# Performance work log

Measured on AMD Instinct MI355X. Metric: run time of the kernel, lower is better.

## Reference

```python
import jax, jax.numpy as jnp
import numpy as np

N_NODES = 30000
N_REL = 8
N_EDGES = 150000
EMB = 128
HID = 128
OUT = 256
HEADS = 4
RANK = 8
SCALE = 1.0
NEG_SLOPE = 0.2
LN_EPS = 1e-5


def setup_inputs():
    key = jax.random.key(0)
    ks = jax.random.split(key, 16)
    def nrm(k, shp, s=0.05):
        return jax.random.normal(k, shp, dtype=jnp.float32) * s
    d2 = HEADS * HID  # conv2 input dim = 512
    return {
        "entity_emb": nrm(ks[0], (N_NODES, EMB)),
        "A1": nrm(ks[1], (N_REL, EMB * RANK)),
        "B1": nrm(ks[2], (N_REL, EMB * RANK)),
        "W1": nrm(ks[3], (HEADS * HID, EMB)),
        "att_l1": nrm(ks[4], (1, HEADS, HID)),
        "att_r1": nrm(ks[5], (1, HEADS, HID)),
        "relb1": jnp.zeros((N_REL, HEADS), jnp.float32),
        "bias1": jnp.zeros((HEADS * HID,), jnp.float32),
        "A2": nrm(ks[6], (N_REL, d2 * RANK)),
        "B2": nrm(ks[7], (N_REL, d2 * RANK)),
        "W2": nrm(ks[8], (OUT, d2)),
        "att_l2": nrm(ks[9], (1, 1, OUT)),
        "att_r2": nrm(ks[10], (1, 1, OUT)),
        "relb2": jnp.zeros((N_REL, 1), jnp.float32),
        "bias2": jnp.zeros((OUT,), jnp.float32),
        "res_W": nrm(ks[11], (OUT, EMB)),
        "res_b": jnp.zeros((OUT,), jnp.float32),
        "ln_g": jnp.ones((OUT,), jnp.float32),
        "ln_b": jnp.zeros((OUT,), jnp.float32),
        "edge_index": jax.random.randint(ks[12], (2, N_EDGES), 0, N_NODES),
        "edge_type": jax.random.randint(ks[13], (N_EDGES,), 0, N_REL),
    }


def _rel_gat_conv(x, A, B, W, att_l, att_r, relb, bias, j_idx, i_idx, etype, heads, out_dim, concat):
    # x: [N,d]; A,B: [R, d*k]; W: [heads*out_dim, d]
    N, d = x.shape
    R = A.shape[0]
    k = RANK
    HC = heads * out_dim
    A3 = A.reshape(R, d, k)
    B3 = B.reshape(R, d, k)
    z_all = x @ W.T  # [N, HC] base linear (shared by z_i and z_j)
    # LoRA low-rank projection per (node, relation): P[n,r] = B_r^T x_n
    P = jnp.einsum('nd,rdk->nrk', x, B3)          # [N,R,k] (small)
    low = P[j_idx, etype]                          # [E,k]
    # Fused LoRA-through-lin: lin(scale*A_r B_r^T x) = scale * low @ (A_r^T W^T)
    M = jnp.einsum('rdk,hd->rkh', A3, W).reshape(R * k, HC)  # [R*k, HC]
    oh = jax.nn.one_hot(etype, R, dtype=x.dtype)   # [E,R]
    low_exp = (oh[:, :, None] * low[:, None, :]).reshape(-1, R * k)  # [E,R*k]
    z_j = (z_all[j_idx] + SCALE * (low_exp @ M)).reshape(-1, heads, out_dim)  # [E,H,C]
    z_i = z_all[i_idx].reshape(-1, heads, out_dim)                            # [E,H,C]
    alpha = (z_i * att_l).sum(-1) + (z_j * att_r).sum(-1) + relb[etype]       # [E,H]
    alpha = jax.nn.leaky_relu(alpha, NEG_SLOPE)
    # per-relation loop => softmax groups are (relation, target node)
    seg = etype * N + i_idx
    n_seg = R * N
    amax = jax.ops.segment_max(alpha, seg, num_segments=n_seg)
    ex = jnp.exp(alpha - amax[seg])
    den = jax.ops.segment_sum(ex, seg, num_segments=n_seg)
    alpha = ex / den[seg]
    msg = z_j * alpha[:, :, None]                  # [E,H,C]
    out = jax.ops.segment_sum(msg, i_idx, num_segments=N)  # [N,H,C]
    out = out.reshape(N, HC) if concat else out.mean(axis=1)
    return out + bias


def _forward(entity_emb, A1, B1, W1, att_l1, att_r1, relb1, bias1,
             A2, B2, W2, att_l2, att_r2, relb2, bias2,
             res_W, res_b, ln_g, ln_b, edge_index, edge_type):
    j_idx, i_idx = edge_index[0], edge_index[1]
    x0 = entity_emb
    x = _rel_gat_conv(x0, A1, B1, W1, att_l1, att_r1, relb1, bias1,
                      j_idx, i_idx, edge_type, HEADS, HID, True)
    x = jax.nn.elu(x)
    x = _rel_gat_conv(x, A2, B2, W2, att_l2, att_r2, relb2, bias2,
                      j_idx, i_idx, edge_type, 1, OUT, False)
    x = x + (x0 @ res_W.T + res_b)
    mu = x.mean(axis=-1, keepdims=True)
    var = ((x - mu) ** 2).mean(axis=-1, keepdims=True)
    return (x - mu) / jnp.sqrt(var + LN_EPS) * ln_g + ln_b


def reference(entity_emb, A1, B1, W1, att_l1, att_r1, relb1, bias1,
              A2, B2, W2, att_l2, att_r2, relb2, bias2,
              res_W, res_b, ln_g, ln_b, edge_index, edge_type):
    return _forward(entity_emb, A1, B1, W1, att_l1, att_r1, relb1, bias1,
                    A2, B2, W2, att_l2, att_r2, relb2, bias2,
                    res_W, res_b, ln_g, ln_b, edge_index, edge_type)
```

## Files before the change

kernel.cpp:

```cpp
#include <hip/hip_runtime.h>
#include <cstddef>

#define NRELS 8
#define EMB 128
#define HID 128
#define OUTD 256
#define HEADS 4
#define RANK 8
#define D2 512
#define KCAT 192
#define NEG_SLOPE 0.2f
#define LN_EPS 1e-5f

typedef short bf16x8 __attribute__((ext_vector_type(8)));
typedef float f32x4 __attribute__((ext_vector_type(4)));

__device__ __forceinline__ unsigned short f2bf(float f) {
  union { float f; unsigned u; } v; v.f = f;
  unsigned u = v.u;
  return (unsigned short)((u + 0x7fffu + ((u >> 16) & 1u)) >> 16);
}
__device__ __forceinline__ float bf2f(unsigned short u) {
  union { unsigned u; float f; } v; v.u = (unsigned)u << 16; return v.f;
}

#define GLOAD16(ldsp, gp) \
  __builtin_amdgcn_global_load_lds((const __attribute__((address_space(1))) unsigned int*)(gp), \
      (__attribute__((address_space(3))) unsigned int*)(ldsp), 16, 0, 0)

template<int ATT, int BIAS, int F32OUT>
__global__ __launch_bounds__(256) void gemm_tile(const unsigned short* __restrict__ A,
    const unsigned short* __restrict__ B, unsigned short* __restrict__ C,
    float* __restrict__ Cf, int M, int N, int K,
    const float* __restrict__ bias, const float* __restrict__ b1p,
    const float* __restrict__ attL, const float* __restrict__ attR,
    float* __restrict__ al, float* __restrict__ ar) {
  __shared__ unsigned short As[128 * 32];
  __shared__ unsigned short Bs[128 * 32];
  __shared__ float pL[2][128];
  __shared__ float pR[2][128];
  const int tid = threadIdx.x;
  const int wave = tid >> 6;
  const int lane = tid & 63;
  const int wm = wave & 1;
  const int wn = wave >> 1;
  const int r16 = lane & 15;
  const int quad = lane >> 4;
  const int bm = blockIdx.x * 128;
  const int bn = blockIdx.y * 128;
  const int lr = lane >> 2;
  const int lc = (((lane & 3) ^ ((lane >> 3) & 3))) * 8;
  int arow0 = bm + wave * 32 + lr;      if (arow0 >= M) arow0 = M - 1;
  int arow1 = bm + wave * 32 + 16 + lr; if (arow1 >= M) arow1 = M - 1;
  const unsigned short* Ag0 = A + (size_t)arow0 * K + lc;
  const unsigned short* Ag1 = A + (size_t)arow1 * K + lc;
  const unsigned short* Bg0 = B + (size_t)(bn + wave * 32 + lr) * K + lc;
  const unsigned short* Bg1 = B + (size_t)(bn + wave * 32 + 16 + lr) * K + lc;
  unsigned short* lA0 = As + wave * 1024;
  unsigned short* lA1 = As + wave * 1024 + 512;
  unsigned short* lB0 = Bs + wave * 1024;
  unsigned short* lB1 = Bs + wave * 1024 + 512;
  const int rsw = (quad ^ ((r16 >> 1) & 3)) * 8;
  f32x4 acc[4][4] = {};
  for (int k0 = 0; k0 < K; k0 += 32) {
    __syncthreads();
    GLOAD16(lA0, Ag0 + k0);
    GLOAD16(lA1, Ag1 + k0);
    GLOAD16(lB0, Bg0 + k0);
    GLOAD16(lB1, Bg1 + k0);
    __syncthreads();
    bf16x8 af[4], bfr[4];
#pragma unroll
    for (int mi = 0; mi < 4; ++mi)
      af[mi] = *(const bf16x8*)(As + (wm * 64 + mi * 16 + r16) * 32 + rsw);
#pragma unroll
    for (int ni = 0; ni < 4; ++ni)
      bfr[ni] = *(const bf16x8*)(Bs + (wn * 64 + ni * 16 + r16) * 32 + rsw);
#pragma unroll
    for (int mi = 0; mi < 4; ++mi)
#pragma unroll
      for (int ni = 0; ni < 4; ++ni)
        acc[mi][ni] = __builtin_amdgcn_mfma_f32_16x16x32_bf16(af[mi], bfr[ni], acc[mi][ni], 0, 0, 0);
  }
  float bcol[4];
  if (BIAS) {
#pragma unroll
    for (int ni = 0; ni < 4; ++ni) {
      int cn = bn + wn * 64 + ni * 16 + r16;
      bcol[ni] = bias[cn];
      if (F32OUT) bcol[ni] += b1p[cn];
    }
  }
#pragma unroll
  for (int mi = 0; mi < 4; ++mi)
#pragma unroll
    for (int ni = 0; ni < 4; ++ni)
#pragma unroll
      for (int r = 0; r < 4; ++r) {
        int row = bm + wm * 64 + mi * 16 + quad * 4 + r;
        if (row < M) {
          float v = acc[mi][ni][r];
          if (BIAS) v += bcol[ni];
          size_t idx = (size_t)row * N + bn + wn * 64 + ni * 16 + r16;
          if (F32OUT) Cf[idx] = v;
          else        C[idx] = f2bf(v);
        }
      }
  if (ATT) {
    float La[4], Ra[4];
#pragma unroll
    for (int ni = 0; ni < 4; ++ni) {
      int cn = bn + wn * 64 + ni * 16 + r16;
      La[ni] = attL[cn]; Ra[ni] = attR[cn];
    }
#pragma unroll
    for (int mi = 0; mi < 4; ++mi)
#pragma unroll
      for (int r = 0; r < 4; ++r) {
        float sl = 0.f, sr = 0.f;
#pragma unroll
        for (int ni = 0; ni < 4; ++ni) {
          sl = fmaf(acc[mi][ni][r], La[ni], sl);
          sr = fmaf(acc[mi][ni][r], Ra[ni], sr);
        }
#pragma unroll
        for (int o = 1; o < 16; o <<= 1) {
          sl += __shfl_xor(sl, o, 64);
          sr += __shfl_xor(sr, o, 64);
        }
        if (r16 == 0) {
          int rl = wm * 64 + mi * 16 + quad * 4 + r;
          pL[wn][rl] = sl; pR[wn][rl] = sr;
        }
      }
    __syncthreads();
    if (tid < 128) {
      int row = bm + tid;
      if (row < M) {
        float sl = pL[0][tid] + pL[1][tid];
        float sr = pR[0][tid] + pR[1][tid];
        if (ATT == 1) {
          al[(size_t)row * 4 + blockIdx.y] = sl;
          ar[(size_t)row * 4 + blockIdx.y] = sr;
        } else {
          al[(size_t)blockIdx.y * M + row] = sl;
          ar[(size_t)blockIdx.y * M + row] = sr;
        }
      }
    }
  }
}

__global__ __launch_bounds__(256) void gemm_bf16t(const unsigned short* __restrict__ A,
    const unsigned short* __restrict__ B, float* __restrict__ C, int M, int N, int K) {
  __shared__ unsigned short As[64][40];
  __shared__ unsigned short Bs[64][40];
  const int tid = threadIdx.x;
  const int wave = tid >> 6;
  const int lane = tid & 63;
  const int wm = wave & 1;
  const int wn = wave >> 1;
  const int r16 = lane & 15;
  const int quad = lane >> 4;
  const int bm = blockIdx.x * 64;
  const int bn = blockIdx.y * 64;
  const int srow = tid >> 2;
  const int schunk = tid & 3;
  int arow = bm + srow; if (arow >= M) arow = M - 1;
  const unsigned short* Ag = A + (size_t)arow * K + schunk * 8;
  const unsigned short* Bg = B + (size_t)(bn + srow) * K + schunk * 8;
  f32x4 acc[2][2] = {};
  for (int k0 = 0; k0 < K; k0 += 32) {
    bf16x8 av = *(const bf16x8*)(Ag + k0);
    bf16x8 bv = *(const bf16x8*)(Bg + k0);
    __syncthreads();
    *(bf16x8*)(&As[srow][schunk * 8]) = av;
    *(bf16x8*)(&Bs[srow][schunk * 8]) = bv;
    __syncthreads();
    bf16x8 af0 = *(const bf16x8*)(&As[wm * 32 + r16][quad * 8]);
    bf16x8 af1 = *(const bf16x8*)(&As[wm * 32 + 16 + r16][quad * 8]);
    bf16x8 bf0 = *(const bf16x8*)(&Bs[wn * 32 + r16][quad * 8]);
    bf16x8 bf1 = *(const bf16x8*)(&Bs[wn * 32 + 16 + r16][quad * 8]);
    acc[0][0] = __builtin_amdgcn_mfma_f32_16x16x32_bf16(af0, bf0, acc[0][0], 0, 0, 0);
    acc[0][1] = __builtin_amdgcn_mfma_f32_16x16x32_bf16(af0, bf1, acc[0][1], 0, 0, 0);
    acc[1][0] = __builtin_amdgcn_mfma_f32_16x16x32_bf16(af1, bf0, acc[1][0], 0, 0, 0);
    acc[1][1] = __builtin_amdgcn_mfma_f32_16x16x32_bf16(af1, bf1, acc[1][1], 0, 0, 0);
  }
#pragma unroll
  for (int mi = 0; mi < 2; ++mi)
#pragma unroll
    for (int ni = 0; ni < 2; ++ni)
#pragma unroll
      for (int r = 0; r < 4; ++r) {
        int row = bm + wm * 32 + mi * 16 + quad * 4 + r;
        if (row < M)
          C[(size_t)row * N + bn + wn * 32 + ni * 16 + r16] = acc[mi][ni][r];
      }
}

__global__ __launch_bounds__(256) void gemm_abt(const float* __restrict__ A,
    const float* __restrict__ B, float* __restrict__ C, int M, int N, int K) {
  __shared__ float As[32][64];
  __shared__ float Bs[32][64];
  const int tid = threadIdx.x;
  const int bm = blockIdx.y * 64;
  const int bn = blockIdx.x * 64;
  const int tx = tid & 15;
  const int ty = tid >> 4;
  const int lr = tid & 63;
  const int lq = tid >> 6;
  float acc[4][4] = {};
  for (int k0 = 0; k0 < K; k0 += 32) {
#pragma unroll
    for (int s = 0; s < 2; ++s) {
      const int q = lq + s * 4;
      const int gm = bm + lr;
      float4 va = make_float4(0.f, 0.f, 0.f, 0.f);
      if (gm < M) va = *(const float4*)(A + (size_t)gm * K + k0 + q * 4);
      As[q * 4 + 0][lr] = va.x; As[q * 4 + 1][lr] = va.y;
      As[q * 4 + 2][lr] = va.z; As[q * 4 + 3][lr] = va.w;
      const int gn = bn + lr;
      float4 vb = *(const float4*)(B + (size_t)gn * K + k0 + q * 4);
      Bs[q * 4 + 0][lr] = vb.x; Bs[q * 4 + 1][lr] = vb.y;
      Bs[q * 4 + 2][lr] = vb.z; Bs[q * 4 + 3][lr] = vb.w;
    }
    __syncthreads();
#pragma unroll
    for (int kk = 0; kk < 32; ++kk) {
      float a[4], b[4];
#pragma unroll
      for (int i2 = 0; i2 < 4; ++i2) { a[i2] = As[kk][ty * 4 + i2]; b[i2] = Bs[kk][tx * 4 + i2]; }
#pragma unroll
      for (int i2 = 0; i2 < 4; ++i2)
#pragma unroll
        for (int j2 = 0; j2 < 4; ++j2)
          acc[i2][j2] = fmaf(a[i2], b[j2], acc[i2][j2]);
    }
    __syncthreads();
  }
#pragma unroll
  for (int i2 = 0; i2 < 4; ++i2) {
    const int gm = bm + ty * 4 + i2;
    if (gm >= M) continue;
#pragma unroll
    for (int j2 = 0; j2 < 4; ++j2)
      C[(size_t)gm * N + bn + tx * 4 + j2] = acc[i2][j2];
  }
}

__global__ void prep_all(const float* __restrict__ x0, const float* __restrict__ W1,
    const float* __restrict__ W2, const float* __restrict__ res_W,
    const float* __restrict__ A1, const float* __restrict__ A2,
    const float* __restrict__ B1, const float* __restrict__ B2,
    unsigned short* __restrict__ x0b, unsigned short* __restrict__ Acat,
    unsigned short* __restrict__ W1b, unsigned short* __restrict__ W2b,
    unsigned short* __restrict__ RWcat,
    float* __restrict__ Amat1, float* __restrict__ Amat2,
    unsigned short* __restrict__ Bmat1b, unsigned short* __restrict__ Bmat2b, int nx0) {
  int idx = blockIdx.x * 256 + threadIdx.x;
  if (idx < nx0) { unsigned short b = f2bf(x0[idx]); x0b[idx] = b;
    Acat[(size_t)(idx >> 7) * KCAT + (idx & 127)] = b; return; } idx -= nx0;
  if (idx < D2 * EMB) { W1b[idx] = f2bf(W1[idx]); return; } idx -= D2 * EMB;
  if (idx < OUTD * D2) { W2b[idx] = f2bf(W2[idx]); return; } idx -= OUTD * D2;
  if (idx < OUTD * EMB) { RWcat[(size_t)(idx >> 7) * KCAT + (idx & 127)] = f2bf(res_W[idx]); return; } idx -= OUTD * EMB;
  if (idx < 64 * EMB) { int d = idx % EMB, rk = idx / EMB, k = rk & 7, r = rk >> 3;
    Amat1[idx] = A1[(size_t)r * EMB * RANK + (size_t)d * RANK + k]; return; } idx -= 64 * EMB;
  if (idx < 64 * D2) { int d = idx % D2, rk = idx / D2, k = rk & 7, r = rk >> 3;
    Amat2[idx] = A2[(size_t)r * D2 * RANK + (size_t)d * RANK + k]; return; } idx -= 64 * D2;
  if (idx < 64 * EMB) { int d = idx % EMB, rk = idx / EMB, k = rk & 7, r = rk >> 3;
    Bmat1b[idx] = f2bf(B1[(size_t)r * EMB * RANK + (size_t)d * RANK + k]); return; } idx -= 64 * EMB;
  if (idx < 64 * D2) { int d = idx % D2, rk = idx / D2, k = rk & 7, r = rk >> 3;
    Bmat2b[idx] = f2bf(B2[(size_t)r * D2 * RANK + (size_t)d * RANK + k]); }
}

__global__ void fold_att(const float* __restrict__ M1, const float* __restrict__ attR1,
                         const float* __restrict__ M2, const float* __restrict__ attR2,
                         float* __restrict__ Matt1, float* __restrict__ Matt2) {
  int t = threadIdx.x;
  if (blockIdx.x == 0) {
    int h = t & 3, rk = t >> 2;
    float s = 0.f;
    for (int c = 0; c < HID; ++c)
      s = fmaf(M1[(size_t)rk * D2 + h * HID + c], attR1[h * HID + c], s);
    Matt1[rk * 4 + h] = s;
  } else if (t < 64) {
    float s = 0.f;
    for (int c = 0; c < OUTD; ++c) s = fmaf(M2[(size_t)t * OUTD + c], attR2[c], s);
    Matt2[t] = s;
  }
}

__global__ void build_MT(const float* __restrict__ M1, const float* __restrict__ M2,
                         unsigned short* __restrict__ M1T, unsigned short* __restrict__ RWcat) {
  int idx = blockIdx.x * 256 + threadIdx.x;
  if (idx < 512 * 256) {
    int c = idx >> 8, s = idx & 255;
    int h = s >> 6, rk = s & 63;
    float v = ((c >> 7) == h) ? M1[(size_t)rk * D2 + c] : 0.f;
    M1T[idx] = f2bf(v);
  } else {
    idx -= 512 * 256;
    if (idx < 256 * 64) {
      int c = idx >> 6, rk = idx & 63;
      RWcat[(size_t)c * KCAT + 128 + rk] = f2bf(M2[(size_t)rk * OUTD + c]);
    }
  }
}

__global__ void hist_kernel(const int* __restrict__ ii, int* __restrict__ deg,
                            int* __restrict__ prepos, int E) {
  int e = blockIdx.x * blockDim.x + threadIdx.x;
  if (e < E) prepos[e] = atomicAdd(&deg[ii[e]], 1);
}

__global__ __launch_bounds__(1024) void exscan_kernel(const int* __restrict__ deg,
                                                      int* __restrict__ rowstart, int n) {
  __shared__ int wsum[16];
  int t = threadIdx.x;
  int lane = t & 63, wid = t >> 6;
  int carry = 0;
  for (int base = 0; base < n; base += 4096) {
    int i0 = base + t * 4;
    int v0 = 0, v1 = 0, v2 = 0, v3 = 0;
    if (i0 + 3 < n) {
      int4 vv = *(const int4*)(deg + i0);
      v0 = vv.x; v1 = vv.y; v2 = vv.z; v3 = vv.w;
    } else {
      if (i0 < n) v0 = deg[i0];
      if (i0 + 1 < n) v1 = deg[i0 + 1];
      if (i0 + 2 < n) v2 = deg[i0 + 2];
      if (i0 + 3 < n) v3 = deg[i0 + 3];
    }
    int tot = v0 + v1 + v2 + v3;
    int x = tot;
#pragma unroll
    for (int o = 1; o < 64; o <<= 1) {
      int y = __shfl_up(x, o, 64);
      if (lane >= o) x += y;
    }
    if (lane == 63) wsum[wid] = x;
    __syncthreads();
    if (t == 0) {
      int s = carry;
      for (int w2 = 0; w2 < 16; ++w2) { int tmp = wsum[w2]; wsum[w2] = s; s += tmp; }
      carry = s;
    }
    __syncthreads();
    int ex0 = x - tot + wsum[wid];
    if (i0 + 3 < n) {
      int4 ov; ov.x = ex0; ov.y = ex0 + v0; ov.z = ex0 + v0 + v1; ov.w = ex0 + v0 + v1 + v2;
      *(int4*)(rowstart + i0) = ov;
    } else {
      if (i0 < n) rowstart[i0] = ex0;
      if (i0 + 1 < n) rowstart[i0 + 1] = ex0 + v0;
      if (i0 + 2 < n) rowstart[i0 + 2] = ex0 + v0 + v1;
      if (i0 + 3 < n) rowstart[i0 + 3] = ex0 + v0 + v1 + v2;
    }
    __syncthreads();
  }
  if (t == 0) rowstart[n] = carry;
}

__global__ void edge_alpha1(const int* __restrict__ ji, const int* __restrict__ ii,
                            const int* __restrict__ et, const int* __restrict__ rowstart,
                            const int* __restrict__ prepos,
                            const float* __restrict__ P1,
                            const float* __restrict__ al1, const float* __restrict__ ar1,
                            const float* __restrict__ relb1, const float* __restrict__ Matt1,
                            float4* __restrict__ recs1, int E) {
  int e = blockIdx.x * blockDim.x + threadIdx.x;
  if (e >= E) return;
  int j = ji[e], i = ii[e], rt = et[e];
  float4 lo0 = *(const float4*)(P1 + (size_t)j * 64 + rt * 8);
  float4 lo1 = *(const float4*)(P1 + (size_t)j * 64 + rt * 8 + 4);
  float low[RANK] = {lo0.x, lo0.y, lo0.z, lo0.w, lo1.x, lo1.y, lo1.z, lo1.w};
  float4 ali = *(const float4*)(al1 + (size_t)i * 4);
  float4 arj = *(const float4*)(ar1 + (size_t)j * 4);
  float4 rb  = *(const float4*)(relb1 + rt * 4);
  float a0 = ali.x + arj.x + rb.x;
  float a1 = ali.y + arj.y + rb.y;
  float a2 = ali.z + arj.z + rb.z;
  float a3 = ali.w + arj.w + rb.w;
#pragma unroll
  for (int k = 0; k < RANK; ++k) {
    float4 mk = *(const float4*)(Matt1 + ((rt * 8 + k) << 2));
    a0 = fmaf(low[k], mk.x, a0); a1 = fmaf(low[k], mk.y, a1);
    a2 = fmaf(low[k], mk.z, a2); a3 = fmaf(low[k], mk.w, a3);
  }
  a0 = (a0 > 0.f) ? a0 : NEG_SLOPE * a0;
  a1 = (a1 > 0.f) ? a1 : NEG_SLOPE * a1;
  a2 = (a2 > 0.f) ? a2 : NEG_SLOPE * a2;
  a3 = (a3 > 0.f) ? a3 : NEG_SLOPE * a3;
  float e0 = expf(a0), e1 = expf(a1), e2 = expf(a2), e3 = expf(a3);
  float4* rp = recs1 + (size_t)(rowstart[i] + prepos[e]) * 4;
  rp[0] = make_float4(__int_as_float(j), e0, e1, e2);
  rp[1] = make_float4(e3, __int_as_float(rt), low[0], low[1]);
  rp[2] = make_float4(low[2], low[3], low[4], low[5]);
  rp[3] = make_float4(low[6], low[7], 0.f, 0.f);
}

__global__ __launch_bounds__(256) void qden1(float4* __restrict__ recs1,
    const int* __restrict__ rowstart, unsigned short* __restrict__ Q1b, int Nn) {
  __shared__ float denS[4][32];
  const int wid = threadIdx.x >> 6, lane = threadIdx.x & 63;
  const int i = blockIdx.x * 4 + wid;
  if (i >= Nn) return;
  const int rt_mine = lane >> 3, k = lane & 7;
  const int s0 = rowstart[i], deg = rowstart[i + 1] - s0;
  const float* rf = (const float*)recs1;
  float q0 = 0.f, q1 = 0.f, q2 = 0.f, q3 = 0.f;
  float d0 = 0.f, d1 = 0.f, d2 = 0.f, d3 = 0.f;
  float4 a0 = {}, a1 = {};
  float lw = 0.f;
  if (deg > 0) {
    a0 = recs1[(size_t)s0 * 4]; a1 = recs1[(size_t)s0 * 4 + 1];
    lw = rf[(size_t)s0 * 16 + 6 + k];
  }
  for (int p = 0; p < deg; ++p) {
    float4 b0 = a0, b1 = a1; float lwn = lw;
    if (p + 1 < deg) {
      b0 = recs1[(size_t)(s0 + p + 1) * 4]; b1 = recs1[(size_t)(s0 + p + 1) * 4 + 1];
      lwn = rf[(size_t)(s0 + p + 1) * 16 + 6 + k];
    }
    int rt = __float_as_int(a1.y);
    if (rt == rt_mine) {
      q0 = fmaf(a0.y, lw, q0); q1 = fmaf(a0.z, lw, q1);
      q2 = fmaf(a0.w, lw, q2); q3 = fmaf(a1.x, lw, q3);
      d0 += a0.y; d1 += a0.z; d2 += a0.w; d3 += a1.x;
    }
    a0 = b0; a1 = b1; lw = lwn;
  }
  float r0 = (d0 > 0.f) ? 1.f / d0 : 0.f;
  float r1 = (d1 > 0.f) ? 1.f / d1 : 0.f;
  float r2 = (d2 > 0.f) ? 1.f / d2 : 0.f;
  float r3 = (d3 > 0.f) ? 1.f / d3 : 0.f;
  size_t qb = (size_t)i * 256;
  Q1b[qb + lane]       = f2bf(q0 * r0);
  Q1b[qb + 64 + lane]  = f2bf(q1 * r1);
  Q1b[qb + 128 + lane] = f2bf(q2 * r2);
  Q1b[qb + 192 + lane] = f2bf(q3 * r3);
  if (k == 0) {
    denS[wid][rt_mine]      = r0;
    denS[wid][8 + rt_mine]  = r1;
    denS[wid][16 + rt_mine] = r2;
    denS[wid][24 + rt_mine] = r3;
  }
  for (int p = lane; p < deg; p += 64) {
    float4* rp = recs1 + (size_t)(s0 + p) * 4;
    float4 v0 = rp[0]; float4 v1 = rp[1];
    int rt = __float_as_int(v1.y);
    v0.y *= denS[wid][rt];      v0.z *= denS[wid][8 + rt];
    v0.w *= denS[wid][16 + rt]; v1.x *= denS[wid][24 + rt];
    rp[0] = v0; rp[1] = v1;
  }
}

__global__ __launch_bounds__(256) void node_agg1_lite(const float4* __restrict__ recs1,
    const int* __restrict__ rowstart, const unsigned short* __restrict__ z1b,
    const unsigned short* __restrict__ L1b, unsigned short* __restrict__ h1out, int Nn) {
  const int wid = threadIdx.x >> 6;
  const int lane = threadIdx.x & 63;
  const int i = blockIdx.x * 4 + wid;
  if (i >= Nn) return;
  const int s0 = rowstart[i];
  const int deg = rowstart[i + 1] - s0;
  const int c0 = lane * 8;
  const float* rf = (const float*)recs1;
  float acc[8] = {};
  float4 rc = {}, rn = {};
  float w3c = 0.f, w3n = 0.f;
  uint4 zc = {};
  if (deg > 0) {
    rc = recs1[(size_t)s0 * 4];
    w3c = rf[(size_t)s0 * 16 + 4];
    zc = *(const uint4*)(z1b + (size_t)__float_as_int(rc.x) * D2 + c0);
  }
  if (deg > 1) {
    rn = recs1[(size_t)(s0 + 1) * 4];
    w3n = rf[(size_t)(s0 + 1) * 16 + 4];
  }
  for (int p = 0; p < deg; ++p) {
    float4 r2 = rn; float w32 = w3n;
    uint4 zn = zc;
    if (p + 2 < deg) {
      r2 = recs1[(size_t)(s0 + p + 2) * 4];
      w32 = rf[(size_t)(s0 + p + 2) * 16 + 4];
    }
    if (p + 1 < deg)
      zn = *(const uint4*)(z1b + (size_t)__float_as_int(rn.x) * D2 + c0);
    float wlo = (lane & 16) ? rc.z : rc.y;
    float whi = (lane & 16) ? w3c : rc.w;
    float wt = (lane & 32) ? whi : wlo;
    acc[0] = fmaf(wt, bf2f((unsigned short)(zc.x & 0xffff)), acc[0]);
    acc[1] = fmaf(wt, bf2f((unsigned short)(zc.x >> 16)), acc[1]);
    acc[2] = fmaf(wt, bf2f((unsigned short)(zc.y & 0xffff)), acc[2]);
    acc[3] = fmaf(wt, bf2f((unsigned short)(zc.y >> 16)), acc[3]);
    acc[4] = fmaf(wt, bf2f((unsigned short)(zc.z & 0xffff)), acc[4]);
    acc[5] = fmaf(wt, bf2f((unsigned short)(zc.z >> 16)), acc[5]);
    acc[6] = fmaf(wt, bf2f((unsigned short)(zc.w & 0xffff)), acc[6]);
    acc[7] = fmaf(wt, bf2f((unsigned short)(zc.w >> 16)), acc[7]);
    rc = rn; w3c = w3n; rn = r2; w3n = w32; zc = zn;
  }
  uint4 lv = *(const uint4*)(L1b + (size_t)i * D2 + c0);
  unsigned lw[4] = {lv.x, lv.y, lv.z, lv.w};
  unsigned ov[4];
#pragma unroll
  for (int q = 0; q < 4; ++q) {
    float e0 = acc[2 * q]     + bf2f((unsigned short)(lw[q] & 0xffff));
    float e1 = acc[2 * q + 1] + bf2f((unsigned short)(lw[q] >> 16));
    e0 = e0 > 0.f ? e0 : expm1f(e0);
    e1 = e1 > 0.f ? e1 : expm1f(e1);
    ov[q] = (unsigned)f2bf(e0) | ((unsigned)f2bf(e1) << 16);
  }
  *(uint4*)(h1out + (size_t)i * D2 + c0) = make_uint4(ov[0], ov[1], ov[2], ov[3]);
}

__global__ void edge_alpha2(const int* __restrict__ ji, const int* __restrict__ ii,
                            const int* __restrict__ et, const int* __restrict__ rowstart,
                            const int* __restrict__ prepos,
                            const float* __restrict__ P2,
                            const float* __restrict__ al2, const float* __restrict__ ar2,
                            const float* __restrict__ relb2, const float* __restrict__ Matt2,
                            float4* __restrict__ recs2, int E, int Nn) {
  int e = blockIdx.x * blockDim.x + threadIdx.x;
  if (e >= E) return;
  int j = ji[e], i = ii[e], rt = et[e];
  float4 lo0 = *(const float4*)(P2 + (size_t)j * 64 + rt * 8);
  float4 lo1 = *(const float4*)(P2 + (size_t)j * 64 + rt * 8 + 4);
  float low[RANK] = {lo0.x, lo0.y, lo0.z, lo0.w, lo1.x, lo1.y, lo1.z, lo1.w};
  float a = al2[i] + al2[(size_t)Nn + i] + ar2[j] + ar2[(size_t)Nn + j] + relb2[rt];
#pragma unroll
  for (int k = 0; k < RANK; ++k) a = fmaf(low[k], Matt2[rt * RANK + k], a);
  a = (a > 0.f) ? a : NEG_SLOPE * a;
  float ex = expf(a);
  float4* rp = recs2 + (size_t)(rowstart[i] + prepos[e]) * 3;
  rp[0] = make_float4(__int_as_float(j), __int_as_float(rt), ex, low[0]);
  rp[1] = make_float4(low[1], low[2], low[3], low[4]);
  rp[2] = make_float4(low[5], low[6], low[7], 0.f);
}

__global__ __launch_bounds__(256) void qden2(float4* __restrict__ recs2,
    const int* __restrict__ rowstart, unsigned short* __restrict__ Acat, int Nn) {
  __shared__ float denS[4][NRELS];
  const int wid = threadIdx.x >> 6, lane = threadIdx.x & 63;
  const int i = blockIdx.x * 4 + wid;
  if (i >= Nn) return;
  const int rt_mine = lane >> 3, k = lane & 7;
  const int s0 = rowstart[i], deg = rowstart[i + 1] - s0;
  const float* rf = (const float*)recs2;
  float q = 0.f, d = 0.f;
  float4 a0 = {}; float lw = 0.f;
  if (deg > 0) { a0 = recs2[(size_t)s0 * 3]; lw = rf[(size_t)s0 * 12 + 3 + k]; }
  for (int p = 0; p < deg; ++p) {
    float4 b0 = a0; float lwn = lw;
    if (p + 1 < deg) {
      b0 = recs2[(size_t)(s0 + p + 1) * 3];
      lwn = rf[(size_t)(s0 + p + 1) * 12 + 3 + k];
    }
    int rt = __float_as_int(a0.y);
    if (rt == rt_mine) { q = fmaf(a0.z, lw, q); d += a0.z; }
    a0 = b0; lw = lwn;
  }
  float rd = (d > 0.f) ? 1.f / d : 0.f;
  Acat[(size_t)i * KCAT + 128 + lane] = f2bf(q * rd);
  if (k == 0) denS[wid][rt_mine] = rd;
  for (int p = lane; p < deg; p += 64) {
    float* ep = (float*)(recs2 + (size_t)(s0 + p) * 3);
    int rt = __float_as_int(ep[1]);
    ep[2] *= denS[wid][rt];
  }
}

__global__ __launch_bounds__(256) void node_agg2_lite(const float4* __restrict__ recs2,
    const int* __restrict__ rowstart, const unsigned short* __restrict__ z2b,
    const float* __restrict__ o2, const float* __restrict__ ln_g,
    const float* __restrict__ ln_b, float* __restrict__ y, int Nn) {
  const int wid = threadIdx.x >> 6;
  const int lane = threadIdx.x & 63;
  const int i = blockIdx.x * 4 + wid;
  if (i >= Nn) return;
  const int s0 = rowstart[i];
  const int deg = rowstart[i + 1] - s0;
  const int c0 = lane * 4;
  float acc[4] = {};
  float4 rc = {}, rn = {};
  uint2 zc = make_uint2(0u, 0u);
  if (deg > 0) {
    rc = recs2[(size_t)s0 * 3];
    zc = *(const uint2*)(z2b + (size_t)__float_as_int(rc.x) * OUTD + c0);
  }
  if (deg > 1) rn = recs2[(size_t)(s0 + 1) * 3];
  for (int p = 0; p < deg; ++p) {
    float4 r2 = rn;
    uint2 zn = zc;
    if (p + 2 < deg) r2 = recs2[(size_t)(s0 + p + 2) * 3];
    if (p + 1 < deg)
      zn = *(const uint2*)(z2b + (size_t)__float_as_int(rn.x) * OUTD + c0);
    float wt = rc.z;
    acc[0] = fmaf(wt, bf2f((unsigned short)(zc.x & 0xffff)), acc[0]);
    acc[1] = fmaf(wt, bf2f((unsigned short)(zc.x >> 16)), acc[1]);
    acc[2] = fmaf(wt, bf2f((unsigned short)(zc.y & 0xffff)), acc[2]);
    acc[3] = fmaf(wt, bf2f((unsigned short)(zc.y >> 16)), acc[3]);
    rc = rn; rn = r2; zc = zn;
  }
  float4 rsv = *(const float4*)(o2 + (size_t)i * OUTD + c0);
  float vv[4];
  vv[0] = acc[0] + rsv.x;
  vv[1] = acc[1] + rsv.y;
  vv[2] = acc[2] + rsv.z;
  vv[3] = acc[3] + rsv.w;
  float s = vv[0] + vv[1] + vv[2] + vv[3];
  for (int o = 32; o > 0; o >>= 1) s += __shfl_xor(s, o, 64);
  float mu = s * (1.f / OUTD);
  float q = 0.f;
#pragma unroll
  for (int k = 0; k < 4; ++k) { float d = vv[k] - mu; q += d * d; }
  for (int o = 32; o > 0; o >>= 1) q += __shfl_xor(q, o, 64);
  float rstd = rsqrtf(q * (1.f / OUTD) + LN_EPS);
  float4 g = *(const float4*)(ln_g + c0);
  float4 bb = *(const float4*)(ln_b + c0);
  float4 ov;
  ov.x = (vv[0] - mu) * rstd * g.x + bb.x;
  ov.y = (vv[1] - mu) * rstd * g.y + bb.y;
  ov.z = (vv[2] - mu) * rstd * g.z + bb.z;
  ov.w = (vv[3] - mu) * rstd * g.w + bb.w;
  *(float4*)(y + (size_t)i * OUTD + c0) = ov;
}

extern "C" void kernel_launch(void* const* d_in, const int* in_sizes, int n_in,
                              void* d_out, int out_size, void* d_ws, size_t ws_size,
                              hipStream_t stream) {
  const float* x0     = (const float*)d_in[0];
  const float* A1     = (const float*)d_in[1];
  const float* B1     = (const float*)d_in[2];
  const float* W1     = (const float*)d_in[3];
  const float* attL1  = (const float*)d_in[4];
  const float* attR1  = (const float*)d_in[5];
  const float* relb1  = (const float*)d_in[6];
  const float* bias1  = (const float*)d_in[7];
  const float* A2     = (const float*)d_in[8];
  const float* B2     = (const float*)d_in[9];
  const float* W2     = (const float*)d_in[10];
  const float* attL2  = (const float*)d_in[11];
  const float* attR2  = (const float*)d_in[12];
  const float* relb2  = (const float*)d_in[13];
  const float* bias2  = (const float*)d_in[14];
  const float* res_W  = (const float*)d_in[15];
  const float* res_b  = (const float*)d_in[16];
  const float* ln_g   = (const float*)d_in[17];
  const float* ln_b   = (const float*)d_in[18];
  const int*   eidx   = (const int*)d_in[19];
  const int*   etype  = (const int*)d_in[20];
  float* out = (float*)d_out;

  const int Nn = in_sizes[0] / EMB;
  const int E  = in_sizes[20];
  const int* ji = eidx;
  const int* ii = eidx + E;

  float* w = (float*)d_ws;
  size_t off = 0;
  float* o2    = w + off; off += (size_t)Nn * OUTD;
  float* P1    = w + off; off += (size_t)Nn * 64;
  float* P2    = w + off; off += (size_t)Nn * 64;
  float* M1    = w + off; off += 64 * D2;
  float* M2    = w + off; off += 64 * OUTD;
  float* Amat1 = w + off; off += 64 * EMB;
  float* Amat2 = w + off; off += 64 * D2;
  float* Matt1 = w + off; off += 64 * 4;
  float* Matt2 = w + off; off += 64;
  float* al1   = w + off; off += (size_t)Nn * 4;
  float* ar1   = w + off; off += (size_t)Nn * 4;
  float* al2   = w + off; off += (size_t)Nn * 2;
  float* ar2   = w + off; off += (size_t)Nn * 2;
  float4* recs1 = (float4*)(w + off); off += (size_t)E * 16;
  float4* recs2 = (float4*)(w + off); off += (size_t)E * 12;
  unsigned short* z1b    = (unsigned short*)(w + off); off += (size_t)Nn * D2 / 2;
  unsigned short* z2b    = (unsigned short*)(w + off); off += (size_t)Nn * OUTD / 2;
  unsigned short* x0b    = (unsigned short*)(w + off); off += (size_t)Nn * EMB / 2;
  unsigned short* h1b    = (unsigned short*)(w + off); off += (size_t)Nn * D2 / 2;
  unsigned short* W1b    = (unsigned short*)(w + off); off += (size_t)D2 * EMB / 2;
  unsigned short* W2b    = (unsigned short*)(w + off); off += (size_t)OUTD * D2 / 2;
  unsigned short* Bmat1b = (unsigned short*)(w + off); off += (size_t)64 * EMB / 2;
  unsigned short* Bmat2b = (unsigned short*)(w + off); off += (size_t)64 * D2 / 2;
  unsigned short* Acat   = (unsigned short*)(w + off); off += (size_t)Nn * KCAT / 2;
  unsigned short* RWcat  = (unsigned short*)(w + off); off += (size_t)OUTD * KCAT / 2;
  unsigned short* M1T    = (unsigned short*)(w + off); off += (size_t)512 * 256 / 2;
  int* ideg     = (int*)(w + off); off += (size_t)Nn;
  int* prepos   = (int*)(w + off); off += (size_t)E;
  int* rowstart = (int*)(w + off); off += (size_t)Nn + 1;
  (void)ws_size; (void)n_in; (void)out_size;

  unsigned short* Q1b = (unsigned short*)P1;
  unsigned short* L1b = (unsigned short*)o2;

  const int MT64 = (Nn + 63) / 64;
  const int MT128 = (Nn + 127) / 128;
  const int NB4 = (Nn + 3) / 4;

  (void)hipMemsetAsync(ideg, 0, (size_t)Nn * sizeof(int), stream);
  hist_kernel<<<(E + 255) / 256, 256, 0, stream>>>(ii, ideg, prepos, E);
  exscan_kernel<<<1, 1024, 0, stream>>>(ideg, rowstart, Nn);

  {
    int nx0 = Nn * EMB;
    int total = nx0 + D2 * EMB + OUTD * D2 + OUTD * EMB + 64 * EMB + 64 * D2 + 64 * EMB + 64 * D2;
    prep_all<<<(total + 255) / 256, 256, 0, stream>>>(x0, W1, W2, res_W, A1, A2, B1, B2,
        x0b, Acat, W1b, W2b, RWcat, Amat1, Amat2, Bmat1b, Bmat2b, nx0);
  }

  gemm_abt<<<dim3(D2 / 64, 1), 256, 0, stream>>>(Amat1, W1, M1, 64, D2, EMB);
  gemm_abt<<<dim3(OUTD / 64, 1), 256, 0, stream>>>(Amat2, W2, M2, 64, OUTD, D2);
  fold_att<<<2, 256, 0, stream>>>(M1, attR1, M2, attR2, Matt1, Matt2);
  build_MT<<<(512 * 256 + 256 * 64 + 255) / 256, 256, 0, stream>>>(M1, M2, M1T, RWcat);

  gemm_tile<1, 0, 0><<<dim3(MT128, D2 / 128), 256, 0, stream>>>(x0b, W1b, z1b, nullptr,
      Nn, D2, EMB, nullptr, nullptr, attL1, attR1, al1, ar1);
  gemm_bf16t<<<dim3(MT64, 1), 256, 0, stream>>>(x0b, Bmat1b, P1, Nn, 64, EMB);

  edge_alpha1<<<(E + 255) / 256, 256, 0, stream>>>(ji, ii, etype, rowstart, prepos, P1,
                                                   al1, ar1, relb1, Matt1, recs1, E);
  qden1<<<NB4, 256, 0, stream>>>(recs1, rowstart, Q1b, Nn);
  gemm_tile<0, 1, 0><<<dim3(MT128, D2 / 128), 256, 0, stream>>>(Q1b, M1T, L1b, nullptr,
      Nn, D2, 256, bias1, nullptr, nullptr, nullptr, nullptr, nullptr);
  node_agg1_lite<<<NB4, 256, 0, stream>>>(recs1, rowstart, z1b, L1b, h1b, Nn);

  gemm_tile<2, 0, 0><<<dim3(MT128, OUTD / 128), 256, 0, stream>>>(h1b, W2b, z2b, nullptr,
      Nn, OUTD, D2, nullptr, nullptr, attL2, attR2, al2, ar2);
  gemm_bf16t<<<dim3(MT64, 1), 256, 0, stream>>>(h1b, Bmat2b, P2, Nn, 64, D2);

  edge_alpha2<<<(E + 255) / 256, 256, 0, stream>>>(ji, ii, etype, rowstart, prepos, P2,
                                                   al2, ar2, relb2, Matt2, recs2, E, Nn);
  qden2<<<NB4, 256, 0, stream>>>(recs2, rowstart, Acat, Nn);
  gemm_tile<0, 1, 1><<<dim3(MT128, OUTD / 128), 256, 0, stream>>>(Acat, RWcat, nullptr, o2,
      Nn, OUTD, KCAT, bias2, res_b, nullptr, nullptr, nullptr, nullptr);
  node_agg2_lite<<<NB4, 256, 0, stream>>>(recs2, rowstart, z2b, o2, ln_g, ln_b, out, Nn);
}
```

Before: 401.9 us.

## Fuse LoRA projection GEMMs into main GEMMs, exploit block-diagonal M1T, merge prep kernels

Folds the per-node LoRA P projection into the z GEMM launch as an extra grid column, removing separate gemm_bf16t launches. Replaces the block-diagonal 512x256 M1T with a dense 512x64 per-head slice, indexed by a per-column A offset, which cuts the Q1 GEMM K from 256 to 64. Merges the two weight-folding GEMMs into one launch and fold_att with build_MT into one kernel. Deepens the gather prefetch pipeline in both aggregation kernels to two neighbours ahead. Risks include extra register pressure and load imbalance from the narrower P tile.

```diff
diff --git a/kernel.cpp b/kernel.cpp
--- a/kernel.cpp
+++ b/kernel.cpp
@@ -28,10 +28,11 @@
   __builtin_amdgcn_global_load_lds((const __attribute__((address_space(1))) unsigned int*)(gp), \
       (__attribute__((address_space(3))) unsigned int*)(ldsp), 16, 0, 0)
 
-template<int ATT, int BIAS, int F32OUT>
+template<int ATT, int BIAS, int F32OUT, int PB>
 __global__ __launch_bounds__(256) void gemm_tile(const unsigned short* __restrict__ A,
     const unsigned short* __restrict__ B, unsigned short* __restrict__ C,
-    float* __restrict__ Cf, int M, int N, int K,
+    float* __restrict__ Cf, const unsigned short* __restrict__ Bp,
+    float* __restrict__ Cp, int M, int N, int K, int lda, int aoffc,
     const float* __restrict__ bias, const float* __restrict__ b1p,
     const float* __restrict__ attL, const float* __restrict__ attR,
     float* __restrict__ al, float* __restrict__ ar) {
@@ -47,20 +48,60 @@
   const int r16 = lane & 15;
   const int quad = lane >> 4;
   const int bm = blockIdx.x * 128;
-  const int bn = blockIdx.y * 128;
   const int lr = lane >> 2;
   const int lc = (((lane & 3) ^ ((lane >> 3) & 3))) * 8;
+  const int rsw = (quad ^ ((r16 >> 1) & 3)) * 8;
   int arow0 = bm + wave * 32 + lr;      if (arow0 >= M) arow0 = M - 1;
   int arow1 = bm + wave * 32 + 16 + lr; if (arow1 >= M) arow1 = M - 1;
-  const unsigned short* Ag0 = A + (size_t)arow0 * K + lc;
-  const unsigned short* Ag1 = A + (size_t)arow1 * K + lc;
+  unsigned short* lA0 = As + wave * 1024;
+  unsigned short* lA1 = As + wave * 1024 + 512;
+
+  if (PB && blockIdx.y == (int)gridDim.y - 1) {
+    const unsigned short* Ag0 = A + (size_t)arow0 * lda + lc;
+    const unsigned short* Ag1 = A + (size_t)arow1 * lda + lc;
+    const unsigned short* Bg = Bp + (size_t)(wave * 16 + lr) * K + lc;
+    unsigned short* lBp = Bs + wave * 512;
+    f32x4 accp[4][2] = {};
+    for (int k0 = 0; k0 < K; k0 += 32) {
+      __syncthreads();
+      GLOAD16(lA0, Ag0 + k0);
+      GLOAD16(lA1, Ag1 + k0);
+      GLOAD16(lBp, Bg + k0);
+      __syncthreads();
+      bf16x8 af[4], bfr[2];
+#pragma unroll
+      for (int mi = 0; mi < 4; ++mi)
+        af[mi] = *(const bf16x8*)(As + (wm * 64 + mi * 16 + r16) * 32 + rsw);
+#pragma unroll
+      for (int ni = 0; ni < 2; ++ni)
+        bfr[ni] = *(const bf16x8*)(Bs + (wn * 32 + ni * 16 + r16) * 32 + rsw);
+#pragma unroll
+      for (int mi = 0; mi < 4; ++mi)
+#pragma unroll
+        for (int ni = 0; ni < 2; ++ni)
+          accp[mi][ni] = __builtin_amdgcn_mfma_f32_16x16x32_bf16(af[mi], bfr[ni], accp[mi][ni], 0, 0, 0);
+    }
+#pragma unroll
+    for (int mi = 0; mi < 4; ++mi)
+#pragma unroll
+      for (int ni = 0; ni < 2; ++ni)
+#pragma unroll
+        for (int r = 0; r < 4; ++r) {
+          int row = bm + wm * 64 + mi * 16 + quad * 4 + r;
+          if (row < M)
+            Cp[(size_t)row * 64 + wn * 32 + ni * 16 + r16] = accp[mi][ni][r];
+        }
+    return;
+  }
+
+  const int bn = blockIdx.y * 128;
+  const unsigned short* Abase = A + (size_t)blockIdx.y * aoffc;
+  const unsigned short* Ag0 = Abase + (size_t)arow0 * lda + lc;
+  const unsigned short* Ag1 = Abase + (size_t)arow1 * lda + lc;
   const unsigned short* Bg0 = B + (size_t)(bn + wave * 32 + lr) * K + lc;
   const unsigned short* Bg1 = B + (size_t)(bn + wave * 32 + 16 + lr) * K + lc;
-  unsigned short* lA0 = As + wave * 1024;
-  unsigned short* lA1 = As + wave * 1024 + 512;
   unsigned short* lB0 = Bs + wave * 1024;
   unsigned short* lB1 = Bs + wave * 1024 + 512;
-  const int rsw = (quad ^ ((r16 >> 1) & 3)) * 8;
   f32x4 acc[4][4] = {};
   for (int k0 = 0; k0 < K; k0 += 32) {
     __syncthreads();
@@ -151,60 +192,15 @@
   }
 }
 
-__global__ __launch_bounds__(256) void gemm_bf16t(const unsigned short* __restrict__ A,
-    const unsigned short* __restrict__ B, float* __restrict__ C, int M, int N, int K) {
-  __shared__ unsigned short As[64][40];
-  __shared__ unsigned short Bs[64][40];
-  const int tid = threadIdx.x;
-  const int wave = tid >> 6;
-  const int lane = tid & 63;
-  const int wm = wave & 1;
-  const int wn = wave >> 1;
-  const int r16 = lane & 15;
-  const int quad = lane >> 4;
-  const int bm = blockIdx.x * 64;
-  const int bn = blockIdx.y * 64;
-  const int srow = tid >> 2;
-  const int schunk = tid & 3;
-  int arow = bm + srow; if (arow >= M) arow = M - 1;
-  const unsigned short* Ag = A + (size_t)arow * K + schunk * 8;
-  const unsigned short* Bg = B + (size_t)(bn + srow) * K + schunk * 8;
-  f32x4 acc[2][2] = {};
-  for (int k0 = 0; k0 < K; k0 += 32) {
-    bf16x8 av = *(const bf16x8*)(Ag + k0);
-    bf16x8 bv = *(const bf16x8*)(Bg + k0);
-    __syncthreads();
-    *(bf16x8*)(&As[srow][schunk * 8]) = av;
-    *(bf16x8*)(&Bs[srow][schunk * 8]) = bv;
-    __syncthreads();
-    bf16x8 af0 = *(const bf16x8*)(&As[wm * 32 + r16][quad * 8]);
-    bf16x8 af1 = *(const bf16x8*)(&As[wm * 32 + 16 + r16][quad * 8]);
-    bf16x8 bf0 = *(const bf16x8*)(&Bs[wn * 32 + r16][quad * 8]);
-    bf16x8 bf1 = *(const bf16x8*)(&Bs[wn * 32 + 16 + r16][quad * 8]);
-    acc[0][0] = __builtin_amdgcn_mfma_f32_16x16x32_bf16(af0, bf0, acc[0][0], 0, 0, 0);
-    acc[0][1] = __builtin_amdgcn_mfma_f32_16x16x32_bf16(af0, bf1, acc[0][1], 0, 0, 0);
-    acc[1][0] = __builtin_amdgcn_mfma_f32_16x16x32_bf16(af1, bf0, acc[1][0], 0, 0, 0);
-    acc[1][1] = __builtin_amdgcn_mfma_f32_16x16x32_bf16(af1, bf1, acc[1][1], 0, 0, 0);
-  }
-#pragma unroll
-  for (int mi = 0; mi < 2; ++mi)
-#pragma unroll
-    for (int ni = 0; ni < 2; ++ni)
-#pragma unroll
-      for (int r = 0; r < 4; ++r) {
-        int row = bm + wm * 32 + mi * 16 + quad * 4 + r;
-        if (row < M)
-          C[(size_t)row * N + bn + wn * 32 + ni * 16 + r16] = acc[mi][ni][r];
-      }
-}
-
-__global__ __launch_bounds__(256) void gemm_abt(const float* __restrict__ A,
-    const float* __restrict__ B, float* __restrict__ C, int M, int N, int K) {
+__global__ __launch_bounds__(256) void gemm_abt2(const float* __restrict__ Amat1,
+    const float* __restrict__ W1, float* __restrict__ M1o,
+    const float* __restrict__ Amat2, const float* __restrict__ W2, float* __restrict__ M2o) {
+  const float* A; const float* B; float* C; int N, K, bn;
+  if (blockIdx.x < D2 / 64) { A = Amat1; B = W1; C = M1o; N = D2; K = EMB; bn = blockIdx.x * 64; }
+  else { A = Amat2; B = W2; C = M2o; N = OUTD; K = D2; bn = (blockIdx.x - D2 / 64) * 64; }
   __shared__ float As[32][64];
   __shared__ float Bs[32][64];
   const int tid = threadIdx.x;
-  const int bm = blockIdx.y * 64;
-  const int bn = blockIdx.x * 64;
   const int tx = tid & 15;
   const int ty = tid >> 4;
   const int lr = tid & 63;
@@ -214,13 +210,10 @@
 #pragma unroll
     for (int s = 0; s < 2; ++s) {
       const int q = lq + s * 4;
-      const int gm = bm + lr;
-      float4 va = make_float4(0.f, 0.f, 0.f, 0.f);
-      if (gm < M) va = *(const float4*)(A + (size_t)gm * K + k0 + q * 4);
+      float4 va = *(const float4*)(A + (size_t)lr * K + k0 + q * 4);
       As[q * 4 + 0][lr] = va.x; As[q * 4 + 1][lr] = va.y;
       As[q * 4 + 2][lr] = va.z; As[q * 4 + 3][lr] = va.w;
-      const int gn = bn + lr;
-      float4 vb = *(const float4*)(B + (size_t)gn * K + k0 + q * 4);
+      float4 vb = *(const float4*)(B + (size_t)(bn + lr) * K + k0 + q * 4);
       Bs[q * 4 + 0][lr] = vb.x; Bs[q * 4 + 1][lr] = vb.y;
       Bs[q * 4 + 2][lr] = vb.z; Bs[q * 4 + 3][lr] = vb.w;
     }
@@ -239,13 +232,10 @@
     __syncthreads();
   }
 #pragma unroll
-  for (int i2 = 0; i2 < 4; ++i2) {
-    const int gm = bm + ty * 4 + i2;
-    if (gm >= M) continue;
+  for (int i2 = 0; i2 < 4; ++i2)
 #pragma unroll
     for (int j2 = 0; j2 < 4; ++j2)
-      C[(size_t)gm * N + bn + tx * 4 + j2] = acc[i2][j2];
-  }
+      C[(size_t)(ty * 4 + i2) * N + bn + tx * 4 + j2] = acc[i2][j2];
 }
 
 __global__ void prep_all(const float* __restrict__ x0, const float* __restrict__ W1,
@@ -273,38 +263,24 @@
     Bmat2b[idx] = f2bf(B2[(size_t)r * D2 * RANK + (size_t)d * RANK + k]); }
 }
 
-__global__ void fold_att(const float* __restrict__ M1, const float* __restrict__ attR1,
-                         const float* __restrict__ M2, const float* __restrict__ attR2,
-                         float* __restrict__ Matt1, float* __restrict__ Matt2) {
-  int t = threadIdx.x;
-  if (blockIdx.x == 0) {
-    int h = t & 3, rk = t >> 2;
+__global__ void fold_build(const float* __restrict__ M1, const float* __restrict__ M2,
+                           const float* __restrict__ attR1, const float* __restrict__ attR2,
+                           unsigned short* __restrict__ M1T2, unsigned short* __restrict__ RWcat,
+                           float* __restrict__ Matt1, float* __restrict__ Matt2) {
+  int idx = blockIdx.x * 256 + threadIdx.x;
+  if (idx < 512 * 64) { int c = idx >> 6, rk = idx & 63;
+    M1T2[idx] = f2bf(M1[(size_t)rk * D2 + c]); return; } idx -= 512 * 64;
+  if (idx < 256 * 64) { int c = idx >> 6, rk = idx & 63;
+    RWcat[(size_t)c * KCAT + 128 + rk] = f2bf(M2[(size_t)rk * OUTD + c]); return; } idx -= 256 * 64;
+  if (idx < 256) { int h = idx & 3, rk = idx >> 2;
     float s = 0.f;
     for (int c = 0; c < HID; ++c)
       s = fmaf(M1[(size_t)rk * D2 + h * HID + c], attR1[h * HID + c], s);
-    Matt1[rk * 4 + h] = s;
-  } else if (t < 64) {
+    Matt1[rk * 4 + h] = s; return; } idx -= 256;
+  if (idx < 64) {
     float s = 0.f;
-    for (int c = 0; c < OUTD; ++c) s = fmaf(M2[(size_t)t * OUTD + c], attR2[c], s);
-    Matt2[t] = s;
-  }
-}
-
-__global__ void build_MT(const float* __restrict__ M1, const float* __restrict__ M2,
-                         unsigned short* __restrict__ M1T, unsigned short* __restrict__ RWcat) {
-  int idx = blockIdx.x * 256 + threadIdx.x;
-  if (idx < 512 * 256) {
-    int c = idx >> 8, s = idx & 255;
-    int h = s >> 6, rk = s & 63;
-    float v = ((c >> 7) == h) ? M1[(size_t)rk * D2 + c] : 0.f;
-    M1T[idx] = f2bf(v);
-  } else {
-    idx -= 512 * 256;
-    if (idx < 256 * 64) {
-      int c = idx >> 6, rk = idx & 63;
-      RWcat[(size_t)c * KCAT + 128 + rk] = f2bf(M2[(size_t)rk * OUTD + c]);
-    }
-  }
+    for (int c = 0; c < OUTD; ++c) s = fmaf(M2[(size_t)idx * OUTD + c], attR2[c], s);
+    Matt2[idx] = s; }
 }
 
 __global__ void hist_kernel(const int* __restrict__ ii, int* __restrict__ deg,
@@ -467,39 +443,31 @@
   const int c0 = lane * 8;
   const float* rf = (const float*)recs1;
   float acc[8] = {};
-  float4 rc = {}, rn = {};
-  float w3c = 0.f, w3n = 0.f;
-  uint4 zc = {};
-  if (deg > 0) {
-    rc = recs1[(size_t)s0 * 4];
-    w3c = rf[(size_t)s0 * 16 + 4];
-    zc = *(const uint4*)(z1b + (size_t)__float_as_int(rc.x) * D2 + c0);
-  }
-  if (deg > 1) {
-    rn = recs1[(size_t)(s0 + 1) * 4];
-    w3n = rf[(size_t)(s0 + 1) * 16 + 4];
-  }
+  float4 r0 = {}, r1 = {}, r2 = {};
+  float w0 = 0.f, w1 = 0.f, w2 = 0.f;
+  uint4 za = {}, zb = {};
+  if (deg > 0) { r0 = recs1[(size_t)s0 * 4]; w0 = rf[(size_t)s0 * 16 + 4];
+    za = *(const uint4*)(z1b + (size_t)__float_as_int(r0.x) * D2 + c0); }
+  if (deg > 1) { r1 = recs1[(size_t)(s0 + 1) * 4]; w1 = rf[(size_t)(s0 + 1) * 16 + 4];
+    zb = *(const uint4*)(z1b + (size_t)__float_as_int(r1.x) * D2 + c0); }
+  if (deg > 2) { r2 = recs1[(size_t)(s0 + 2) * 4]; w2 = rf[(size_t)(s0 + 2) * 16 + 4]; }
   for (int p = 0; p < deg; ++p) {
-    float4 r2 = rn; float w32 = w3n;
-    uint4 zn = zc;
-    if (p + 2 < deg) {
-      r2 = recs1[(size_t)(s0 + p + 2) * 4];
-      w32 = rf[(size_t)(s0 + p + 2) * 16 + 4];
-    }
-    if (p + 1 < deg)
-      zn = *(const uint4*)(z1b + (size_t)__float_as_int(rn.x) * D2 + c0);
-    float wlo = (lane & 16) ? rc.z : rc.y;
-    float whi = (lane & 16) ? w3c : rc.w;
+    float4 r3 = r2; float w3 = w2; uint4 zn = zb;
+    if (p + 3 < deg) { r3 = recs1[(size_t)(s0 + p + 3) * 4];
+                       w3 = rf[(size_t)(s0 + p + 3) * 16 + 4]; }
+    if (p + 2 < deg) zn = *(const uint4*)(z1b + (size_t)__float_as_int(r2.x) * D2 + c0);
+    float wlo = (lane & 16) ? r0.z : r0.y;
+    float whi = (lane & 16) ? w0 : r0.w;
     float wt = (lane & 32) ? whi : wlo;
-    acc[0] = fmaf(wt, bf2f((unsigned short)(zc.x & 0xffff)), acc[0]);
-    acc[1] = fmaf(wt, bf2f((unsigned short)(zc.x >> 16)), acc[1]);
-    acc[2] = fmaf(wt, bf2f((unsigned short)(zc.y & 0xffff)), acc[2]);
-    acc[3] = fmaf(wt, bf2f((unsigned short)(zc.y >> 16)), acc[3]);
-    acc[4] = fmaf(wt, bf2f((unsigned short)(zc.z & 0xffff)), acc[4]);
-    acc[5] = fmaf(wt, bf2f((unsigned short)(zc.z >> 16)), acc[5]);
-    acc[6] = fmaf(wt, bf2f((unsigned short)(zc.w & 0xffff)), acc[6]);
-    acc[7] = fmaf(wt, bf2f((unsigned short)(zc.w >> 16)), acc[7]);
-    rc = rn; w3c = w3n; rn = r2; w3n = w32; zc = zn;
+    acc[0] = fmaf(wt, bf2f((unsigned short)(za.x & 0xffff)), acc[0]);
+    acc[1] = fmaf(wt, bf2f((unsigned short)(za.x >> 16)), acc[1]);
+    acc[2] = fmaf(wt, bf2f((unsigned short)(za.y & 0xffff)), acc[2]);
+    acc[3] = fmaf(wt, bf2f((unsigned short)(za.y >> 16)), acc[3]);
+    acc[4] = fmaf(wt, bf2f((unsigned short)(za.z & 0xffff)), acc[4]);
+    acc[5] = fmaf(wt, bf2f((unsigned short)(za.z >> 16)), acc[5]);
+    acc[6] = fmaf(wt, bf2f((unsigned short)(za.w & 0xffff)), acc[6]);
+    acc[7] = fmaf(wt, bf2f((unsigned short)(za.w >> 16)), acc[7]);
+    r0 = r1; w0 = w1; r1 = r2; w1 = w2; r2 = r3; w2 = w3; za = zb; zb = zn;
   }
   uint4 lv = *(const uint4*)(L1b + (size_t)i * D2 + c0);
   unsigned lw[4] = {lv.x, lv.y, lv.z, lv.w};
@@ -583,25 +551,25 @@
   const int deg = rowstart[i + 1] - s0;
   const int c0 = lane * 4;
   float acc[4] = {};
-  float4 rc = {}, rn = {};
-  uint2 zc = make_uint2(0u, 0u);
-  if (deg > 0) {
-    rc = recs2[(size_t)s0 * 3];
-    zc = *(const uint2*)(z2b + (size_t)__float_as_int(rc.x) * OUTD + c0);
-  }
-  if (deg > 1) rn = recs2[(size_t)(s0 + 1) * 3];
+  float4 r0 = {}, r1 = {}, r2 = {};
+  uint2 za = make_uint2(0u, 0u), zb = make_uint2(0u, 0u);
+  if (deg > 0) { r0 = recs2[(size_t)s0 * 3];
+    za = *(const uint2*)(z2b + (size_t)__float_as_int(r0.x) * OUTD + c0); }
+  if (deg > 1) { r1 = recs2[(size_t)(s0 + 1) * 3];
+    zb = *(const uint2*)(z2b + (size_t)__float_as_int(r1.x) * OUTD + c0); }
+  if (deg > 2) r2 = recs2[(size_t)(s0 + 2) * 3];
   for (int p = 0; p < deg; ++p) {
-    float4 r2 = rn;
-    uint2 zn = zc;
-    if (p + 2 < deg) r2 = recs2[(size_t)(s0 + p + 2) * 3];
-    if (p + 1 < deg)
-      zn = *(const uint2*)(z2b + (size_t)__float_as_int(rn.x) * OUTD + c0);
-    float wt = rc.z;
-    acc[0] = fmaf(wt, bf2f((unsigned short)(zc.x & 0xffff)), acc[0]);
-    acc[1] = fmaf(wt, bf2f((unsigned short)(zc.x >> 16)), acc[1]);
-    acc[2] = fmaf(wt, bf2f((unsigned short)(zc.y & 0xffff)), acc[2]);
-    acc[3] = fmaf(wt, bf2f((unsigned short)(zc.y >> 16)), acc[3]);
-    rc = rn; rn = r2; zc = zn;
+    float4 r3 = r2;
+    uint2 zn = zb;
+    if (p + 3 < deg) r3 = recs2[(size_t)(s0 + p + 3) * 3];
+    if (p + 2 < deg)
+      zn = *(const uint2*)(z2b + (size_t)__float_as_int(r2.x) * OUTD + c0);
+    float wt = r0.z;
+    acc[0] = fmaf(wt, bf2f((unsigned short)(za.x & 0xffff)), acc[0]);
+    acc[1] = fmaf(wt, bf2f((unsigned short)(za.x >> 16)), acc[1]);
+    acc[2] = fmaf(wt, bf2f((unsigned short)(za.y & 0xffff)), acc[2]);
+    acc[3] = fmaf(wt, bf2f((unsigned short)(za.y >> 16)), acc[3]);
+    r0 = r1; r1 = r2; r2 = r3; za = zb; zb = zn;
   }
   float4 rsv = *(const float4*)(o2 + (size_t)i * OUTD + c0);
   float vv[4];
@@ -685,7 +653,7 @@
   unsigned short* Bmat2b = (unsigned short*)(w + off); off += (size_t)64 * D2 / 2;
   unsigned short* Acat   = (unsigned short*)(w + off); off += (size_t)Nn * KCAT / 2;
   unsigned short* RWcat  = (unsigned short*)(w + off); off += (size_t)OUTD * KCAT / 2;
-  unsigned short* M1T    = (unsigned short*)(w + off); off += (size_t)512 * 256 / 2;
+  unsigned short* M1T2   = (unsigned short*)(w + off); off += (size_t)512 * 64 / 2;
   int* ideg     = (int*)(w + off); off += (size_t)Nn;
   int* prepos   = (int*)(w + off); off += (size_t)E;
   int* rowstart = (int*)(w + off); off += (size_t)Nn + 1;
@@ -694,7 +662,6 @@
   unsigned short* Q1b = (unsigned short*)P1;
   unsigned short* L1b = (unsigned short*)o2;
 
-  const int MT64 = (Nn + 63) / 64;
   const int MT128 = (Nn + 127) / 128;
   const int NB4 = (Nn + 3) / 4;
 
@@ -709,30 +676,27 @@
         x0b, Acat, W1b, W2b, RWcat, Amat1, Amat2, Bmat1b, Bmat2b, nx0);
   }
 
-  gemm_abt<<<dim3(D2 / 64, 1), 256, 0, stream>>>(Amat1, W1, M1, 64, D2, EMB);
-  gemm_abt<<<dim3(OUTD / 64, 1), 256, 0, stream>>>(Amat2, W2, M2, 64, OUTD, D2);
-  fold_att<<<2, 256, 0, stream>>>(M1, attR1, M2, attR2, Matt1, Matt2);
-  build_MT<<<(512 * 256 + 256 * 64 + 255) / 256, 256, 0, stream>>>(M1, M2, M1T, RWcat);
-
-  gemm_tile<1, 0, 0><<<dim3(MT128, D2 / 128), 256, 0, stream>>>(x0b, W1b, z1b, nullptr,
-      Nn, D2, EMB, nullptr, nullptr, attL1, attR1, al1, ar1);
-  gemm_bf16t<<<dim3(MT64, 1), 256, 0, stream>>>(x0b, Bmat1b, P1, Nn, 64, EMB);
+  gemm_abt2<<<dim3(D2 / 64 + OUTD / 64, 1), 256, 0, stream>>>(Amat1, W1, M1, Amat2, W2, M2);
+  fold_build<<<(512 * 64 + 256 * 64 + 256 + 64 + 255) / 256, 256, 0, stream>>>(
+      M1, M2, attR1, attR2, M1T2, RWcat, Matt1, Matt2);
+
+  gemm_tile<1, 0, 0, 1><<<dim3(MT128, D2 / 128 + 1), 256, 0, stream>>>(x0b, W1b, z1b, nullptr,
+      Bmat1b, P1, Nn, D2, EMB, EMB, 0, nullptr, nullptr, attL1, attR1, al1, ar1);
 
   edge_alpha1<<<(E + 255) / 256, 256, 0, stream>>>(ji, ii, etype, rowstart, prepos, P1,
                                                    al1, ar1, relb1, Matt1, recs1, E);
   qden1<<<NB4, 256, 0, stream>>>(recs1, rowstart, Q1b, Nn);
-  gemm_tile<0, 1, 0><<<dim3(MT128, D2 / 128), 256, 0, stream>>>(Q1b, M1T, L1b, nullptr,
-      Nn, D2, 256, bias1, nullptr, nullptr, nullptr, nullptr, nullptr);
+  gemm_tile<0, 1, 0, 0><<<dim3(MT128, D2 / 128), 256, 0, stream>>>(Q1b, M1T2, L1b, nullptr,
+      nullptr, nullptr, Nn, D2, 64, 256, 64, bias1, nullptr, nullptr, nullptr, nullptr, nullptr);
   node_agg1_lite<<<NB4, 256, 0, stream>>>(recs1, rowstart, z1b, L1b, h1b, Nn);
 
-  gemm_tile<2, 0, 0><<<dim3(MT128, OUTD / 128), 256, 0, stream>>>(h1b, W2b, z2b, nullptr,
-      Nn, OUTD, D2, nullptr, nullptr, attL2, attR2, al2, ar2);
-  gemm_bf16t<<<dim3(MT64, 1), 256, 0, stream>>>(h1b, Bmat2b, P2, Nn, 64, D2);
+  gemm_tile<2, 0, 0, 1><<<dim3(MT128, OUTD / 128 + 1), 256, 0, stream>>>(h1b, W2b, z2b, nullptr,
+      Bmat2b, P2, Nn, OUTD, D2, D2, 0, nullptr, nullptr, attL2, attR2, al2, ar2);
 
   edge_alpha2<<<(E + 255) / 256, 256, 0, stream>>>(ji, ii, etype, rowstart, prepos, P2,
                                                    al2, ar2, relb2, Matt2, recs2, E, Nn);
   qden2<<<NB4, 256, 0, stream>>>(recs2, rowstart, Acat, Nn);
-  gemm_tile<0, 1, 1><<<dim3(MT128, OUTD / 128), 256, 0, stream>>>(Acat, RWcat, nullptr, o2,
-      Nn, OUTD, KCAT, bias2, res_b, nullptr, nullptr, nullptr, nullptr);
+  gemm_tile<0, 1, 1, 0><<<dim3(MT128, OUTD / 128), 256, 0, stream>>>(Acat, RWcat, nullptr, o2,
+      nullptr, nullptr, Nn, OUTD, KCAT, KCAT, 0, bias2, res_b, nullptr, nullptr, nullptr, nullptr);
   node_agg2_lite<<<NB4, 256, 0, stream>>>(recs2, rowstart, z2b, o2, ln_g, ln_b, out, Nn);
 }
```

Measured after the change: 366.4 us. -8.8%, faster.
